# Performance work log

Measured on AMD Instinct MI355X. Metric: run time of the kernel, lower is better.

## Reference

```python
import jax, jax.numpy as jnp
import numpy as np

TOP_K = 2

def setup_inputs() -> dict:
    key = jax.random.key(0)
    ks = jax.random.split(key, 8)
    B, S, H, E, F = 4, 2048, 1024, 8, 2048  # F = hidden * expansion(2)
    scale_in = 0.02
    return {
        "x": jax.random.normal(ks[0], (B, S, H), dtype=jnp.float32),
        "router_w": jax.random.normal(ks[1], (H, E), dtype=jnp.float32) * scale_in,
        "router_b": jnp.zeros((E,), dtype=jnp.float32),
        "w1": jax.random.normal(ks[2], (E, H, F), dtype=jnp.float32) * scale_in,
        "b1": jnp.zeros((E, F), dtype=jnp.float32),
        "w2": jax.random.normal(ks[3], (E, F, H), dtype=jnp.float32) * scale_in,
        "b2": jnp.zeros((E, H), dtype=jnp.float32),
    }

def reference(x, router_w, router_b, w1, b1, w2, b2):
    B, S, H = x.shape
    E = router_b.shape[0]
    T = B * S
    flat = x.reshape(T, H)
    # Router + top-k gating (softmax over the k selected logits, as in torch code)
    logits = flat @ router_w + router_b                       # [T, E]
    topk_scores, topk_idx = jax.lax.top_k(logits, TOP_K)      # [T, k]
    probs = jax.nn.softmax(topk_scores, axis=-1)              # [T, k]
    # Dense gate matrix: gates[t, e] = prob if e selected for token t else 0
    gates = jnp.zeros((T, E), dtype=flat.dtype).at[
        jnp.arange(T)[:, None], topk_idx
    ].add(probs)                                              # [T, E]
    # Expert FFNs computed as batched GEMMs over the expert axis
    h = jax.nn.relu(jnp.einsum('td,edf->etf', flat, w1) + b1[:, None, :])  # [E, T, F]
    eout = jnp.einsum('etf,efd->etd', h, w2) + b2[:, None, :]              # [E, T, H]
    out = jnp.einsum('etd,te->td', eout, gates)                            # [T, H]
    return out.reshape(B, S, H)
```

## Files before the change

kernel.cpp:

```cpp
#include <hip/hip_runtime.h>
#include <hip/hip_bf16.h>

#define T_TOK 8192
#define HDIM 1024
#define FDIM 2048
#define NEXP 8
#define NASSIGN (T_TOK * 2)
#define ROWCAP (NASSIGN + 256)
#define NHB 64
#define MAXT 136

typedef __bf16 bf16;
typedef __bf16 bf16x4 __attribute__((ext_vector_type(4)));
typedef __bf16 bf16x8 __attribute__((ext_vector_type(8)));
typedef float f32x4 __attribute__((ext_vector_type(4)));

__device__ __forceinline__ void gload_lds16(const void* g, void* l) {
    __builtin_amdgcn_global_load_lds(
        (const __attribute__((address_space(1))) void*)(uintptr_t)g,
        (__attribute__((address_space(3))) void*)(uintptr_t)l,
        16, 0, 0);
}

__global__ __launch_bounds__(256) void transpose_to_bf16(
    const float* __restrict__ in, bf16* __restrict__ out, int R, int C) {
    __shared__ float tile[64][68];
    int e = blockIdx.z;
    const float* inp = in + (size_t)e * R * C;
    bf16* outp = out + (size_t)e * R * C;
    int c0 = blockIdx.x * 64, r0 = blockIdx.y * 64;
    int tid = threadIdx.x;
    int tx = tid & 15, ty = tid >> 4;
#pragma unroll
    for (int i = 0; i < 4; i++) {
        int row = ty + i * 16;
        float4 v = *(const float4*)&inp[(size_t)(r0 + row) * C + c0 + tx * 4];
        *(float4*)&tile[row][tx * 4] = v;
    }
    __syncthreads();
#pragma unroll
    for (int i = 0; i < 2; i++) {
        int idx = tid + i * 256;
        int c = idx >> 3, seg = idx & 7;
        bf16x8 v;
#pragma unroll
        for (int j = 0; j < 8; j++) v[j] = (bf16)tile[seg * 8 + j][c];
        *(bf16x8*)&outp[(size_t)(c0 + c) * R + r0 + seg * 8] = v;
    }
}

__global__ __launch_bounds__(256) void router_kernel(
    const float* __restrict__ x, const float* __restrict__ rw,
    const float* __restrict__ rb, int* __restrict__ expert_pair,
    float2* __restrict__ gate_pair) {
    __shared__ float rwT[NEXP][HDIM];
    __shared__ float rbs[NEXP];
    int tid = threadIdx.x;
    for (int i = tid; i < HDIM * NEXP / 4; i += 256) {
        float4 v = ((const float4*)rw)[i];
        int h = i >> 1, e0 = (i & 1) * 4;
        rwT[e0 + 0][h] = v.x;
        rwT[e0 + 1][h] = v.y;
        rwT[e0 + 2][h] = v.z;
        rwT[e0 + 3][h] = v.w;
    }
    if (tid < NEXP) rbs[tid] = rb[tid];
    __syncthreads();
    int wave = tid >> 6, lane = tid & 63;
    int tbase = blockIdx.x * 32 + wave * 8;

    for (int tk = 0; tk < 8; tk++) {
        int t = tbase + tk;
        const float4* xt = (const float4*)(x + (size_t)t * HDIM);
        float p[NEXP];
#pragma unroll
        for (int e = 0; e < NEXP; e++) p[e] = 0.f;
#pragma unroll
        for (int it = 0; it < 4; it++) {
            float4 v = xt[it * 64 + lane];
            int h = (it * 64 + lane) * 4;
#pragma unroll
            for (int e = 0; e < NEXP; e++) {
                float4 wv = *(const float4*)&rwT[e][h];
                p[e] += v.x * wv.x + v.y * wv.y + v.z * wv.z + v.w * wv.w;
            }
        }
#pragma unroll
        for (int off = 32; off >= 1; off >>= 1) {
#pragma unroll
            for (int e = 0; e < NEXP; e++) p[e] += __shfl_xor(p[e], off, 64);
        }
        if (lane == 0) {
            float lg[NEXP];
#pragma unroll
            for (int e = 0; e < NEXP; e++) lg[e] = p[e] + rbs[e];
            int e0 = 0;
#pragma unroll
            for (int e = 1; e < NEXP; e++)
                if (lg[e] > lg[e0]) e0 = e;
            int e1 = -1;
#pragma unroll
            for (int e = 0; e < NEXP; e++) {
                if (e == e0) continue;
                if (e1 < 0 || lg[e] > lg[e1]) e1 = e;
            }
            float z = expf(lg[e1] - lg[e0]);
            expert_pair[t] = e0 | (e1 << 16);
            gate_pair[t] = make_float2(1.f / (1.f + z), z / (1.f + z));
        }
    }
}

__global__ __launch_bounds__(256) void hist_kernel(
    const int* __restrict__ expert_pair, int* __restrict__ hist) {
    int tid = threadIdx.x;
    int wave = tid >> 6, lane = tid & 63;
    int a = blockIdx.x * 256 + tid;
    int t = a >> 1, j = a & 1;
    int e = (expert_pair[t] >> (16 * j)) & 0xffff;
    __shared__ int wcnt[4][NEXP];
#pragma unroll
    for (int ee = 0; ee < NEXP; ee++) {
        unsigned long long m = __ballot(e == ee);
        if (lane == 0) wcnt[wave][ee] = __popcll(m);
    }
    __syncthreads();
    if (tid < NEXP)
        hist[blockIdx.x * NEXP + tid] =
            wcnt[0][tid] + wcnt[1][tid] + wcnt[2][tid] + wcnt[3][tid];
}

__global__ __launch_bounds__(256) void scan_kernel(
    const int* __restrict__ hist, int* __restrict__ start,
    int* __restrict__ cnt, int* __restrict__ offs,
    int* __restrict__ tile_e, int* __restrict__ tile_m,
    int* __restrict__ ntiles) {
    __shared__ int h[NHB * NEXP];
    __shared__ int tot[NEXP];
    __shared__ int offsh[NEXP];
    int tid = threadIdx.x;
    for (int i = tid; i < NHB * NEXP; i += 256) h[i] = hist[i];
    __syncthreads();
    if (tid < NEXP) {
        int s = 0;
        for (int b = 0; b < NHB; b++) s += h[b * NEXP + tid];
        tot[tid] = s;
        cnt[tid] = s;
    }
    __syncthreads();
    if (tid == 0) {
        int o = 0;
        for (int e = 0; e < NEXP; e++) {
            offsh[e] = o;
            offs[e] = o;
            o += tot[e];
        }
        int idx = 0;
        for (int e = 0; e < NEXP; e++) {
            int nt = (tot[e] + 127) >> 7;
            for (int m = 0; m < nt; m++) {
                tile_e[idx] = e;
                tile_m[idx] = m;
                idx++;
            }
        }
        ntiles[0] = idx;
    }
    __syncthreads();
    if (tid < NEXP) {
        int run = offsh[tid];
        for (int b = 0; b < NHB; b++) {
            start[b * NEXP + tid] = run;
            run += h[b * NEXP + tid];
        }
    }
}

__global__ __launch_bounds__(256) void scatter_kernel(
    const int* __restrict__ expert_pair, const float2* __restrict__ gate_pair,
    const int* __restrict__ start, int* __restrict__ perm,
    float* __restrict__ gatebuf, int* __restrict__ rowbuf) {
    int tid = threadIdx.x;
    int wave = tid >> 6, lane = tid & 63;
    int a = blockIdx.x * 256 + tid;
    int t = a >> 1, j = a & 1;
    int e = (expert_pair[t] >> (16 * j)) & 0xffff;
    float2 gp = gate_pair[t];
    float g = j ? gp.y : gp.x;
    __shared__ int wcnt[4][NEXP];
    int rankw = 0;
    unsigned long long below = (1ull << lane) - 1ull;
#pragma unroll
    for (int ee = 0; ee < NEXP; ee++) {
        unsigned long long m = __ballot(e == ee);
        if (lane == 0) wcnt[wave][ee] = __popcll(m);
        if (ee == e) rankw = __popcll(m & below);
    }
    __syncthreads();
    int cross = 0;
    for (int w = 0; w < wave; w++) cross += wcnt[w][e];
    int pos = start[blockIdx.x * NEXP + e] + cross + rankw;
    perm[pos] = t;
    gatebuf[pos] = g;
    rowbuf[a] = pos;
}

__global__ __launch_bounds__(256) void pack_kernel(
    const float* __restrict__ x, const int* __restrict__ perm,
    bf16* __restrict__ xg) {
    int r0 = blockIdx.x * 16;
    int wave = threadIdx.x >> 6, lane = threadIdx.x & 63;
#pragma unroll
    for (int i = 0; i < 4; i++) {
        int row = r0 + wave * 4 + i;
        int tok = perm[row];
        const float* src = x + (size_t)tok * HDIM;
        bf16* dst = xg + (size_t)row * HDIM;
#pragma unroll
        for (int it = 0; it < 4; it++) {
            int c = (it * 64 + lane) * 4;
            float4 v = *(const float4*)&src[c];
            bf16x4 b = {(bf16)v.x, (bf16)v.y, (bf16)v.z, (bf16)v.w};
            *(bf16x4*)&dst[c] = b;
        }
    }
}

template <bool RELU, bool GATE, int NT>
__global__ __launch_bounds__(256, 2) void moe_gemm(
    const bf16* __restrict__ A, const bf16* __restrict__ B,
    const float* __restrict__ bias, const float* __restrict__ gates,
    bf16* __restrict__ out, const int* __restrict__ cnt,
    const int* __restrict__ offs, const int* __restrict__ tile_e,
    const int* __restrict__ tile_m, const int* __restrict__ ntiles,
    int K, int N) {
    int ntl = ntiles[0];
    int nact = ntl * NT;
    int f = blockIdx.x;
    if (f >= nact) return;
    int q = nact >> 3, r = nact & 7;
    int xcd = f & 7, rest = f >> 3;
    int wg = (xcd < r) ? (xcd * (q + 1) + rest)
                       : (r * (q + 1) + (xcd - r) * q + rest);
    int tile = wg / NT;
    int ncol = wg - tile * NT;
    int e = tile_e[tile];
    int n_cnt = cnt[e];
    int off_e = offs[e];
    int m0 = tile_m[tile] * 128;
    int n0 = ncol * 128;

    __shared__ bf16 As[2 * 128 * 64];
    __shared__ bf16 Bs[2 * 128 * 64];

    int tid = threadIdx.x;
    int lane = tid & 63;
    int wave = tid >> 6;
    int wm = (wave & 1) * 64, wn = (wave >> 1) * 64;
    int quad = lane >> 4;
    int l16 = lane & 15;

    const bf16* Ae = A + (size_t)off_e * K;
    const bf16* Be = B + (size_t)e * N * K;

    int srow = lane >> 3;
    int sseg = (lane & 7) ^ srow;
    const bf16* ag = Ae + (size_t)(m0 + wave * 8 + srow) * K + sseg * 8;
    const bf16* bg = Be + (size_t)(n0 + wave * 8 + srow) * K + sseg * 8;
    bf16* al = As + wave * 8 * 64;
    bf16* bl = Bs + wave * 8 * 64;

    auto stage = [&](int buf, int kt) {
        const bf16* a = ag + (size_t)kt * 64;
        const bf16* b = bg + (size_t)kt * 64;
        bf16* la = al + buf * (128 * 64);
        bf16* lb = bl + buf * (128 * 64);
#pragma unroll
        for (int i = 0; i < 4; i++) {
            gload_lds16(a + (size_t)(i * 32) * K, la + i * 32 * 64);
            gload_lds16(b + (size_t)(i * 32) * K, lb + i * 32 * 64);
        }
    };

    f32x4 acc[4][4];
#pragma unroll
    for (int i = 0; i < 4; i++)
#pragma unroll
        for (int j = 0; j < 4; j++) acc[i][j] = f32x4{0.f, 0.f, 0.f, 0.f};

    int nk = K >> 6;
    int swz = l16 & 7;

    stage(0, 0);
    stage(1, 1);
    asm volatile("s_waitcnt vmcnt(8)" ::: "memory");
    asm volatile("s_barrier" ::: "memory");

    for (int kt = 0; kt < nk; kt++) {
        int cur = kt & 1;
        const bf16* ac = As + cur * (128 * 64);
        const bf16* bc = Bs + cur * (128 * 64);
#pragma unroll
        for (int kk = 0; kk < 2; kk++) {
            int sg = ((kk * 4 + quad) ^ swz) * 8;
            bf16x8 af[4], bfr[4];
#pragma unroll
            for (int i = 0; i < 4; i++)
                af[i] = *(const bf16x8*)&ac[(wm + i * 16 + l16) * 64 + sg];
#pragma unroll
            for (int j = 0; j < 4; j++)
                bfr[j] = *(const bf16x8*)&bc[(wn + j * 16 + l16) * 64 + sg];
#pragma unroll
            for (int i = 0; i < 4; i++)
#pragma unroll
                for (int j = 0; j < 4; j++)
                    acc[i][j] = __builtin_amdgcn_mfma_f32_16x16x32_bf16(
                        af[i], bfr[j], acc[i][j], 0, 0, 0);
        }
        asm volatile("s_barrier" ::: "memory");
        if (kt + 2 < nk) {
            stage(cur, kt + 2);
            asm volatile("s_waitcnt vmcnt(8)" ::: "memory");
        } else {
            asm volatile("s_waitcnt vmcnt(0)" ::: "memory");
        }
        asm volatile("s_barrier" ::: "memory");
    }

#pragma unroll
    for (int i = 0; i < 4; i++)
#pragma unroll
        for (int j = 0; j < 4; j++)
#pragma unroll
            for (int r2 = 0; r2 < 4; r2++) {
                int m = m0 + wm + i * 16 + quad * 4 + r2;
                if (m < n_cnt) {
                    int n = n0 + wn + j * 16 + l16;
                    float v = acc[i][j][r2] + bias[e * N + n];
                    if (RELU) v = v > 0.f ? v : 0.f;
                    if (GATE) v *= gates[off_e + m];
                    out[(size_t)(off_e + m) * N + n] = (bf16)v;
                }
            }
}

__global__ __launch_bounds__(256) void combine_kernel(
    const bf16* __restrict__ eout, const int* __restrict__ rowbuf,
    float* __restrict__ out) {
    int t = blockIdx.x;
    int r0 = rowbuf[2 * t], r1 = rowbuf[2 * t + 1];
    const bf16* p0 = eout + (size_t)r0 * HDIM;
    const bf16* p1 = eout + (size_t)r1 * HDIM;
    float* o = out + (size_t)t * HDIM;
    int n = threadIdx.x * 4;
    bf16x4 a = *(const bf16x4*)&p0[n];
    bf16x4 b = *(const bf16x4*)&p1[n];
    float4 v = {(float)a[0] + (float)b[0], (float)a[1] + (float)b[1],
                (float)a[2] + (float)b[2], (float)a[3] + (float)b[3]};
    *(float4*)&o[n] = v;
}

extern "C" void kernel_launch(void* const* d_in, const int* in_sizes, int n_in,
                              void* d_out, int out_size, void* d_ws, size_t ws_size,
                              hipStream_t stream) {
    const float* x = (const float*)d_in[0];
    const float* rw = (const float*)d_in[1];
    const float* rb = (const float*)d_in[2];
    const float* w1 = (const float*)d_in[3];
    const float* b1 = (const float*)d_in[4];
    const float* w2 = (const float*)d_in[5];
    const float* b2 = (const float*)d_in[6];
    float* out = (float*)d_out;

    char* ws = (char*)d_ws;
    size_t o = 0;
    auto alloc = [&](size_t bytes) {
        char* p = ws + o;
        o += (bytes + 255) & ~(size_t)255;
        return p;
    };
    bf16* w1t = (bf16*)alloc((size_t)NEXP * FDIM * HDIM * 2);
    bf16* w2t = (bf16*)alloc((size_t)NEXP * HDIM * FDIM * 2);
    bf16* hbuf = (bf16*)alloc((size_t)ROWCAP * FDIM * 2);
    bf16* xg = (bf16*)alloc((size_t)ROWCAP * HDIM * 2);
    bf16* eout = xg;
    int* expert_pair = (int*)alloc((size_t)T_TOK * 4);
    float2* gate_pair = (float2*)alloc((size_t)T_TOK * 8);
    int* hist = (int*)alloc((size_t)NHB * NEXP * 4);
    int* start = (int*)alloc((size_t)NHB * NEXP * 4);
    int* perm = (int*)alloc((size_t)NASSIGN * 4);
    float* gatebuf = (float*)alloc((size_t)NASSIGN * 4);
    int* rowbuf = (int*)alloc((size_t)NASSIGN * 4);
    int* cnt = (int*)alloc(256);
    int* offs = (int*)alloc(256);
    int* tile_e = (int*)alloc((size_t)MAXT * 4);
    int* tile_m = (int*)alloc((size_t)MAXT * 4);
    int* ntiles = (int*)alloc(256);

    transpose_to_bf16<<<dim3(FDIM / 64, HDIM / 64, NEXP), 256, 0, stream>>>(w1, w1t, HDIM, FDIM);
    transpose_to_bf16<<<dim3(HDIM / 64, FDIM / 64, NEXP), 256, 0, stream>>>(w2, w2t, FDIM, HDIM);
    router_kernel<<<T_TOK / 32, 256, 0, stream>>>(x, rw, rb, expert_pair, gate_pair);
    hist_kernel<<<NHB, 256, 0, stream>>>(expert_pair, hist);
    scan_kernel<<<1, 256, 0, stream>>>(hist, start, cnt, offs, tile_e, tile_m, ntiles);
    scatter_kernel<<<NHB, 256, 0, stream>>>(expert_pair, gate_pair, start, perm, gatebuf, rowbuf);
    pack_kernel<<<NASSIGN / 16, 256, 0, stream>>>(x, perm, xg);
    moe_gemm<true, false, FDIM / 128><<<dim3(MAXT * (FDIM / 128)), 256, 0, stream>>>(
        xg, w1t, b1, nullptr, hbuf, cnt, offs, tile_e, tile_m, ntiles, HDIM, FDIM);
    moe_gemm<false, true, HDIM / 128><<<dim3(MAXT * (HDIM / 128)), 256, 0, stream>>>(
        hbuf, w2t, b2, gatebuf, eout, cnt, offs, tile_e, tile_m, ntiles, FDIM, HDIM);
    combine_kernel<<<T_TOK, 256, 0, stream>>>(eout, rowbuf, out);
}
```

Baseline: 469.3 us.

## Use 256x256 eight-wave pipelined GEMM for first expert FFN layer

Replaces the first expert GEMM (x @ w1 with ReLU) with a new kernel using 256x256 output tiles, 512 threads, and a phased double-buffered schedule. The schedule interleaves async global-to-LDS loads of A/B half-tiles with MFMA quadrants and raises wave priority around the MFMAs. The scan kernel now also builds a second tile list at 256-row granularity. Larger tiles raise arithmetic intensity and cut redundant weight reads. The cost is more padding waste on partial expert tiles and fewer workgroups to fill the GPU.

```diff
diff --git a/kernel.cpp b/kernel.cpp
--- a/kernel.cpp
+++ b/kernel.cpp
@@ -9,6 +9,7 @@
 #define ROWCAP (NASSIGN + 256)
 #define NHB 64
 #define MAXT 136
+#define MAXT2 72
 
 typedef __bf16 bf16;
 typedef __bf16 bf16x4 __attribute__((ext_vector_type(4)));
@@ -134,7 +135,8 @@
     const int* __restrict__ hist, int* __restrict__ start,
     int* __restrict__ cnt, int* __restrict__ offs,
     int* __restrict__ tile_e, int* __restrict__ tile_m,
-    int* __restrict__ ntiles) {
+    int* __restrict__ ntiles, int* __restrict__ tile_e2,
+    int* __restrict__ tile_m2, int* __restrict__ ntiles2) {
     __shared__ int h[NHB * NEXP];
     __shared__ int tot[NEXP];
     __shared__ int offsh[NEXP];
@@ -165,6 +167,16 @@
             }
         }
         ntiles[0] = idx;
+        int idx2 = 0;
+        for (int e = 0; e < NEXP; e++) {
+            int nt = (tot[e] + 255) >> 8;
+            for (int m = 0; m < nt; m++) {
+                tile_e2[idx2] = e;
+                tile_m2[idx2] = m;
+                idx2++;
+            }
+        }
+        ntiles2[0] = idx2;
     }
     __syncthreads();
     if (tid < NEXP) {
@@ -224,6 +236,139 @@
             *(bf16x4*)&dst[c] = b;
         }
     }
+}
+
+#define QUADC(D, MSUB, NSUB)                                                          \
+    do {                                                                              \
+        bf16x8 af[4][2], bfv[2][2];                                                   \
+        _Pragma("unroll") for (int i = 0; i < 4; i++)                                 \
+            _Pragma("unroll") for (int kk = 0; kk < 2; kk++)                          \
+                af[i][kk] = *(const bf16x8*)&As[D][MSUB][wm * 64 + i * 16 + l16]      \
+                                                [((kk * 4 + quad) ^ swz) * 8];        \
+        _Pragma("unroll") for (int j = 0; j < 2; j++)                                 \
+            _Pragma("unroll") for (int kk = 0; kk < 2; kk++)                          \
+                bfv[j][kk] = *(const bf16x8*)&Bs[D][NSUB][wn * 32 + j * 16 + l16]     \
+                                                 [((kk * 4 + quad) ^ swz) * 8];       \
+        __builtin_amdgcn_s_setprio(1);                                                \
+        _Pragma("unroll") for (int i = 0; i < 4; i++)                                 \
+            _Pragma("unroll") for (int j = 0; j < 2; j++)                             \
+                _Pragma("unroll") for (int kk = 0; kk < 2; kk++)                      \
+                    acc[(MSUB)*4 + i][(NSUB)*2 + j] =                                 \
+                        __builtin_amdgcn_mfma_f32_16x16x32_bf16(                      \
+                            af[i][kk], bfv[j][kk], acc[(MSUB)*4 + i][(NSUB)*2 + j],   \
+                            0, 0, 0);                                                 \
+        __builtin_amdgcn_s_setprio(0);                                                \
+    } while (0)
+
+__global__ __launch_bounds__(512, 2) void moe_gemm1_8ph(
+    const bf16* __restrict__ A, const bf16* __restrict__ B,
+    const float* __restrict__ bias, bf16* __restrict__ out,
+    const int* __restrict__ cnt, const int* __restrict__ offs,
+    const int* __restrict__ tile_e2, const int* __restrict__ tile_m2,
+    const int* __restrict__ ntiles2) {
+    const int K = HDIM, N = FDIM, NT = FDIM / 256;
+    int ntl = ntiles2[0];
+    int nact = ntl * NT;
+    int f = blockIdx.x;
+    if (f >= nact) return;
+    int q8 = nact >> 3, r8 = nact & 7;
+    int xcd = f & 7, rest = f >> 3;
+    int wg = (xcd < r8) ? (xcd * (q8 + 1) + rest)
+                        : (r8 * (q8 + 1) + (xcd - r8) * q8 + rest);
+    int tile = wg / NT, ncol = wg - tile * NT;
+    int e = tile_e2[tile];
+    int n_cnt = cnt[e];
+    int off_e = offs[e];
+    int m0 = tile_m2[tile] * 256;
+    int n0 = ncol * 256;
+
+    __shared__ bf16 As[2][2][128][64];
+    __shared__ bf16 Bs[2][2][128][64];
+
+    int tid = threadIdx.x;
+    int lane = tid & 63;
+    int wave = tid >> 6;
+    int wm = wave & 1;
+    int wn = wave >> 1;
+    int quad = lane >> 4, l16 = lane & 15;
+    int swz = l16 & 7;
+
+    const bf16* Ae = A + (size_t)off_e * K;
+    const bf16* Be = B + (size_t)e * N * K;
+
+    int r0t = tid >> 3;
+    int seg = (tid & 7) ^ (r0t & 7);
+    const bf16* aAsrc = Ae + (size_t)(m0 + r0t) * K + seg * 8;
+    const bf16* aBsrc =
+        Be + (size_t)(n0 + ((r0t >> 5) * 64 + (r0t & 31))) * K + seg * 8;
+
+#define STAGE_A(D, H, KT)                                                      \
+    do {                                                                       \
+        _Pragma("unroll") for (int i = 0; i < 2; i++)                          \
+            gload_lds16(aAsrc + ((size_t)((H)*64 + i * 128)) * K + (KT)*64,    \
+                        &As[D][H][i * 64 + wave * 8][0]);                      \
+    } while (0)
+#define STAGE_B(D, H, KT)                                                      \
+    do {                                                                       \
+        _Pragma("unroll") for (int i = 0; i < 2; i++)                          \
+            gload_lds16(aBsrc + ((size_t)((H)*32 + i * 128)) * K + (KT)*64,    \
+                        &Bs[D][H][i * 64 + wave * 8][0]);                      \
+    } while (0)
+
+    f32x4 acc[8][4];
+#pragma unroll
+    for (int i = 0; i < 8; i++)
+#pragma unroll
+        for (int j = 0; j < 4; j++) acc[i][j] = f32x4{0.f, 0.f, 0.f, 0.f};
+
+    const int nk = K / 64;
+    STAGE_A(0, 0, 0);
+    STAGE_B(0, 0, 0);
+    STAGE_A(0, 1, 0);
+    STAGE_B(0, 1, 0);
+
+    for (int kt = 0; kt < nk; kt++) {
+        int d = kt & 1, d2 = d ^ 1;
+        bool nl = (kt + 1 < nk);
+        asm volatile("s_barrier" ::: "memory");
+        if (nl) {
+            STAGE_A(d2, 0, kt + 1);
+            asm volatile("s_waitcnt vmcnt(6)" ::: "memory");
+        } else {
+            asm volatile("s_waitcnt vmcnt(4)" ::: "memory");
+        }
+        asm volatile("s_barrier" ::: "memory");
+        QUADC(d, 0, 0);
+        if (nl) {
+            STAGE_B(d2, 0, kt + 1);
+            asm volatile("s_waitcnt vmcnt(4)" ::: "memory");
+        } else {
+            asm volatile("s_waitcnt vmcnt(0)" ::: "memory");
+        }
+        asm volatile("s_barrier" ::: "memory");
+        QUADC(d, 0, 1);
+        if (nl) STAGE_A(d2, 1, kt + 1);
+        QUADC(d, 1, 0);
+        if (nl) STAGE_B(d2, 1, kt + 1);
+        QUADC(d, 1, 1);
+    }
+
+#pragma unroll
+    for (int mi = 0; mi < 8; mi++)
+#pragma unroll
+        for (int nj = 0; nj < 4; nj++)
+#pragma unroll
+            for (int r = 0; r < 4; r++) {
+                int m = m0 + wm * 128 + mi * 16 + quad * 4 + r;
+                if (m < n_cnt) {
+                    int n = n0 + wn * 64 + nj * 16 + l16;
+                    float v = acc[mi][nj][r] + bias[e * N + n];
+                    v = v > 0.f ? v : 0.f;
+                    out[(size_t)(off_e + m) * N + n] = (bf16)v;
+                }
+            }
+#undef STAGE_A
+#undef STAGE_B
 }
 
 template <bool RELU, bool GATE, int NT>
@@ -396,16 +541,20 @@
     int* tile_e = (int*)alloc((size_t)MAXT * 4);
     int* tile_m = (int*)alloc((size_t)MAXT * 4);
     int* ntiles = (int*)alloc(256);
+    int* tile_e2 = (int*)alloc((size_t)MAXT2 * 4);
+    int* tile_m2 = (int*)alloc((size_t)MAXT2 * 4);
+    int* ntiles2 = (int*)alloc(256);
 
     transpose_to_bf16<<<dim3(FDIM / 64, HDIM / 64, NEXP), 256, 0, stream>>>(w1, w1t, HDIM, FDIM);
     transpose_to_bf16<<<dim3(HDIM / 64, FDIM / 64, NEXP), 256, 0, stream>>>(w2, w2t, FDIM, HDIM);
     router_kernel<<<T_TOK / 32, 256, 0, stream>>>(x, rw, rb, expert_pair, gate_pair);
     hist_kernel<<<NHB, 256, 0, stream>>>(expert_pair, hist);
-    scan_kernel<<<1, 256, 0, stream>>>(hist, start, cnt, offs, tile_e, tile_m, ntiles);
+    scan_kernel<<<1, 256, 0, stream>>>(hist, start, cnt, offs, tile_e, tile_m,
+                                       ntiles, tile_e2, tile_m2, ntiles2);
     scatter_kernel<<<NHB, 256, 0, stream>>>(expert_pair, gate_pair, start, perm, gatebuf, rowbuf);
     pack_kernel<<<NASSIGN / 16, 256, 0, stream>>>(x, perm, xg);
-    moe_gemm<true, false, FDIM / 128><<<dim3(MAXT * (FDIM / 128)), 256, 0, stream>>>(
-        xg, w1t, b1, nullptr, hbuf, cnt, offs, tile_e, tile_m, ntiles, HDIM, FDIM);
+    moe_gemm1_8ph<<<dim3(MAXT2 * (FDIM / 256)), 512, 0, stream>>>(
+        xg, w1t, b1, hbuf, cnt, offs, tile_e2, tile_m2, ntiles2);
     moe_gemm<false, true, HDIM / 128><<<dim3(MAXT * (HDIM / 128)), 256, 0, stream>>>(
         hbuf, w2t, b2, gatebuf, eout, cnt, offs, tile_e, tile_m, ntiles, FDIM, HDIM);
     combine_kernel<<<T_TOK, 256, 0, stream>>>(eout, rowbuf, out);
```

New measurement: 469.2 us. Within noise of the previous version (-0.0%).
